# Kernel optimization log

Hardware: AMD Instinct MI355X
Metric: run time of the kernel (lower is better)

The kernel has to match this reference:

```python
import jax, jax.numpy as jnp
import numpy as np

HIDDEN = 128
GRID = 8
NB = 32.0            # neighborhood_size
CELL = NB / GRID      # cell_size


def setup_inputs() -> dict:
    key = jax.random.key(0)
    k1, k2, k3, k4 = jax.random.split(key, 4)
    N = 1024
    hidden_states = jax.random.normal(k1, (N, HIDDEN), dtype=jnp.float32)
    positions = jax.random.uniform(k2, (N, 2), dtype=jnp.float32) * 100.0
    fan_in = GRID * GRID * HIDDEN
    bound = 1.0 / np.sqrt(fan_in)
    W = jax.random.uniform(k3, (fan_in, HIDDEN), dtype=jnp.float32, minval=-bound, maxval=bound)
    b = jax.random.uniform(k4, (HIDDEN,), dtype=jnp.float32, minval=-bound, maxval=bound)
    return {"hidden_states": hidden_states, "positions": positions, "W": W, "b": b}


def reference(hidden_states, positions, W, b):
    N, H = hidden_states.shape
    G = GRID
    pos = jax.lax.stop_gradient(positions)  # indices carry no gradient (matches torch int())
    # rel[i, j] = positions[j] - positions[i]
    rel = pos[None, :, :] - pos[:, None, :]                      # [N, N, 2]
    half = NB / 2.0
    inside = (jnp.abs(rel[..., 0]) <= half) & (jnp.abs(rel[..., 1]) <= half)
    not_self = ~jnp.eye(N, dtype=bool)
    valid = inside & not_self                                     # [N, N]
    # rel + half is in [0, NB] when inside, so floor == int() truncation
    gx = jnp.clip(jnp.floor((rel[..., 0] + half) / CELL).astype(jnp.int32), 0, G - 1)
    gy = jnp.clip(jnp.floor((rel[..., 1] + half) / CELL).astype(jnp.int32), 0, G - 1)
    cell = gy * G + gx                                            # [N, N], in [0, G*G)
    # invalid pairs go to a dummy cell G*G per pedestrian
    seg = jnp.where(valid, cell, G * G)
    gid = (jnp.arange(N, dtype=jnp.int32)[:, None] * (G * G + 1) + seg).reshape(-1)
    data = jnp.broadcast_to(hidden_states[None, :, :], (N, N, H)).reshape(N * N, H)
    gmax = jax.ops.segment_max(data, gid, num_segments=N * (G * G + 1))  # [N*(G*G+1), H]
    # torch grid starts at zeros and uses maximum -> clamp at 0; empty cells (-inf) -> 0
    grid = jnp.maximum(gmax.reshape(N, G * G + 1, H)[:, : G * G, :], 0.0)  # [N, G*G, H]
    flat = grid.reshape(N, G * G * H)
    return flat @ W + b
```

## Files before the change

kernel.cpp:

```cpp
#include <hip/hip_runtime.h>
#include <hip/hip_bf16.h>

#define N_PED 1024
#define H 128
#define G 8
#define NCELL 64
#define K_TOT 8192
#define HALF_NB 16.0f
#define INV_CELL 0.25f

#define KSPLIT 16
#define KC 512
#define BM 64
#define BK 64
#define NSTAGE 8

typedef __attribute__((ext_vector_type(8))) short bf16x8;
typedef __attribute__((ext_vector_type(4))) float f32x4;

__device__ __forceinline__ unsigned map_f2u(float v) {
    unsigned u = __float_as_uint(v);
    return (u & 0x80000000u) ? ~u : (u | 0x80000000u);
}
__device__ __forceinline__ unsigned pack2x(unsigned ua, unsigned ub) {
    float2 f = {__uint_as_float(ua ^ 0x80000000u),
                __uint_as_float(ub ^ 0x80000000u)};
    union { __hip_bfloat162 h; unsigned u; } cv;
    cv.h = __float22bfloat162_rn(f);
    return cv.u;
}
__device__ __forceinline__ unsigned pack2f(float fa, float fb) {
    float2 f = {fa, fb};
    union { __hip_bfloat162 h; unsigned u; } cv;
    cv.h = __float22bfloat162_rn(f);
    return cv.u;
}
__device__ __forceinline__ void gl_lds16(const void* g, void* l) {
    __builtin_amdgcn_global_load_lds(
        (const __attribute__((address_space(1))) void*)g,
        (__attribute__((address_space(3))) void*)l, 16, 0, 0);
}

__global__ __launch_bounds__(512) void fused_pre(const float* __restrict__ hs,
                                                 const float* __restrict__ pos,
                                                 const float* __restrict__ W,
                                                 ushort* __restrict__ grid,
                                                 ushort* __restrict__ Wt) {
    __shared__ __align__(16) char smem[36872];
    const int tid = threadIdx.x;

    if (blockIdx.x < N_PED) {
        unsigned* lgrid = (unsigned*)smem;
        int*      list  = (int*)(smem + 32768);
        int*      cnt   = (int*)(smem + 36864);
        const int i = blockIdx.x;

        const unsigned iu = 0x80000000u;
        uint4 iv = {iu, iu, iu, iu};
        for (int k = tid; k < NCELL * H / 4; k += 512) ((uint4*)lgrid)[k] = iv;
        if (tid == 0) *cnt = 0;
        __syncthreads();

        const float2 pi = ((const float2*)pos)[i];
        for (int j = tid; j < N_PED; j += 512) {
            float2 pj = ((const float2*)pos)[j];
            float rx = pj.x - pi.x;
            float ry = pj.y - pi.y;
            if (j != i && fabsf(rx) <= HALF_NB && fabsf(ry) <= HALF_NB) {
                int gx = min(G - 1, max(0, (int)floorf((rx + HALF_NB) * INV_CELL)));
                int gy = min(G - 1, max(0, (int)floorf((ry + HALF_NB) * INV_CELL)));
                int slot = atomicAdd(cnt, 1);
                list[slot] = (j << 8) | (gy * G + gx);
            }
        }
        __syncthreads();

        const int n  = *cnt;
        const int c  = tid & 31;
        const int eg = tid >> 5;
        int e  = eg;
        int p0 = (e < n) ? list[e] : -1;
        int p1 = (e + 16 < n) ? list[e + 16] : -1;
        float v0[4] = {};
        if (p0 >= 0) {
            const float* hp = &hs[(p0 >> 8) * H + c];
            v0[0] = hp[0]; v0[1] = hp[32]; v0[2] = hp[64]; v0[3] = hp[96];
        }
        while (p0 >= 0) {
            int p2 = (e + 32 < n) ? list[e + 32] : -1;
            float v1[4] = {};
            if (p1 >= 0) {
                const float* hp = &hs[(p1 >> 8) * H + c];
                v1[0] = hp[0]; v1[1] = hp[32]; v1[2] = hp[64]; v1[3] = hp[96];
            }
            unsigned* gph = &lgrid[(p0 & 255) * H + c];
            atomicMax(gph + 0,  map_f2u(v0[0]));
            atomicMax(gph + 32, map_f2u(v0[1]));
            atomicMax(gph + 64, map_f2u(v0[2]));
            atomicMax(gph + 96, map_f2u(v0[3]));
            e += 16; p0 = p1; p1 = p2;
            v0[0] = v1[0]; v0[1] = v1[1]; v0[2] = v1[2]; v0[3] = v1[3];
        }
        __syncthreads();

        uint2* dst2 = (uint2*)(grid + (size_t)i * K_TOT);
        for (int q = tid; q < K_TOT / 4; q += 512) {
            uint4 a = ((const uint4*)lgrid)[q];
            uint2 o;
            o.x = pack2x(a.x, a.y);
            o.y = pack2x(a.z, a.w);
            dst2[q] = o;
        }
    } else {
        float* tile = (float*)smem;
        const int bw  = blockIdx.x - N_PED;
        const int k0w = bw * 64;

        for (int x = tid; x < 64 * H; x += 512) {
            int r = x >> 7, cc = x & 127;
            tile[r * 129 + cc] = W[(size_t)(k0w + r) * H + cc];
        }
        __syncthreads();

        const int col = tid >> 2;
        const int kh  = (tid & 3) * 16;
        uint tmp[8];
        #pragma unroll
        for (int t = 0; t < 8; ++t)
            tmp[t] = pack2f(tile[(kh + 2 * t) * 129 + col],
                            tile[(kh + 2 * t + 1) * 129 + col]);
        uint4* w0 = (uint4*)(Wt + (size_t)col * K_TOT + k0w + kh);
        w0[0] = *(const uint4*)&tmp[0];
        w0[1] = *(const uint4*)&tmp[4];
    }
}

__global__ __launch_bounds__(512) void gemm_mfma(const ushort* __restrict__ A,
                                                 const ushort* __restrict__ Wt,
                                                 float* __restrict__ part) {
    __shared__ ushort sA[3][BM * BK];
    __shared__ ushort sB[3][H * BK];

    const int bx = blockIdx.x;
    const int mx = 2 * (bx & 7) + ((bx >> 3) & 1);
    const int ky = bx >> 4;
    const int m0 = mx * BM;
    const int k0 = ky * KC;

    const int tid  = threadIdx.x;
    const int wave = tid >> 6;
    const int lane = tid & 63;
    const int ll   = lane & 15;
    const int lh   = lane >> 4;
    const int lr8  = lane >> 3;
    const int cswz = (lane & 7) ^ (lr8 & 7);
    const int wr   = wave >> 2;
    const int wc   = wave & 3;

    const ushort* Abase = A  + (size_t)(m0 + 8 * wave + lr8) * K_TOT + k0 + cswz * 8;
    const ushort* Bbase = Wt + (size_t)(16 * wave + lr8) * K_TOT     + k0 + cswz * 8;

    f32x4 acc[2][2] = {};

#define STAGE(T, BUF)                                                          \
    do {                                                                       \
        gl_lds16(Abase + (T) * BK, &sA[BUF][(8 * wave) * BK]);                 \
        gl_lds16(Bbase + (T) * BK,              &sB[BUF][(16 * wave) * BK]);   \
        gl_lds16(Bbase + (T) * BK + 8 * K_TOT,  &sB[BUF][(16 * wave + 8) * BK]); \
    } while (0)

    STAGE(0, 0);
    STAGE(1, 1);
    asm volatile("s_waitcnt vmcnt(3)" ::: "memory");
    __builtin_amdgcn_s_barrier();

    #pragma unroll
    for (int t = 0; t < NSTAGE; ++t) {
        if (t + 2 < NSTAGE) STAGE(t + 2, (t + 2) % 3);

        const int buf = t % 3;
        #pragma unroll
        for (int ks = 0; ks < 2; ++ks) {
            const int ch = ks * 4 + lh;
            bf16x8 afrag[2], bfrag[2];
            #pragma unroll
            for (int mt = 0; mt < 2; ++mt) {
                int ar = wr * 32 + mt * 16 + ll;
                afrag[mt] = *(const bf16x8*)&sA[buf][ar * BK + ((ch ^ (ar & 7)) * 8)];
            }
            #pragma unroll
            for (int nt = 0; nt < 2; ++nt) {
                int br = wc * 32 + nt * 16 + ll;
                bfrag[nt] = *(const bf16x8*)&sB[buf][br * BK + ((ch ^ (br & 7)) * 8)];
            }
            #pragma unroll
            for (int mt = 0; mt < 2; ++mt)
                #pragma unroll
                for (int nt = 0; nt < 2; ++nt)
                    acc[mt][nt] = __builtin_amdgcn_mfma_f32_16x16x32_bf16(
                        afrag[mt], bfrag[nt], acc[mt][nt], 0, 0, 0);
        }

        if (t + 1 < NSTAGE) {
            if (t + 2 < NSTAGE)
                asm volatile("s_waitcnt vmcnt(3)" ::: "memory");
            else
                asm volatile("s_waitcnt vmcnt(0)" ::: "memory");
            __builtin_amdgcn_s_barrier();
        }
    }
#undef STAGE

    float* dst = part + (size_t)ky * (N_PED * H);
    #pragma unroll
    for (int mt = 0; mt < 2; ++mt)
        #pragma unroll
        for (int nt = 0; nt < 2; ++nt) {
            int col   = wc * 32 + nt * 16 + ll;
            int rbase = m0 + wr * 32 + mt * 16 + lh * 4;
            #pragma unroll
            for (int r = 0; r < 4; ++r)
                dst[(size_t)(rbase + r) * H + col] = acc[mt][nt][r];
        }
}

__global__ __launch_bounds__(128) void reduce_out(const float* __restrict__ part,
                                                  const float* __restrict__ b,
                                                  float* __restrict__ out) {
    const int idx = (blockIdx.x * 128 + threadIdx.x) * 4;
    float4 acc = *(const float4*)&b[idx & (H - 1)];
    #pragma unroll
    for (int s = 0; s < KSPLIT; ++s) {
        float4 p = *(const float4*)&part[(size_t)s * (N_PED * H) + idx];
        acc.x += p.x; acc.y += p.y; acc.z += p.z; acc.w += p.w;
    }
    *(float4*)&out[idx] = acc;
}

extern "C" void kernel_launch(void* const* d_in, const int* in_sizes, int n_in,
                              void* d_out, int out_size, void* d_ws, size_t ws_size,
                              hipStream_t stream) {
    const float* hs  = (const float*)d_in[0];
    const float* pos = (const float*)d_in[1];
    const float* Wm  = (const float*)d_in[2];
    const float* b   = (const float*)d_in[3];
    float* out = (float*)d_out;

    ushort* grid = (ushort*)d_ws;
    ushort* Wt   = (ushort*)((char*)d_ws + (16u << 20));
    float*  part = (float*)((char*)d_ws + (18u << 20));

    fused_pre<<<N_PED + 128, 512, 0, stream>>>(hs, pos, Wm, grid, Wt);
    gemm_mfma<<<KSPLIT * (N_PED / BM), 512, 0, stream>>>(grid, Wt, part);
    reduce_out<<<(N_PED * H) / (128 * 4), 128, 0, stream>>>(part, b, out);
}
```

Before: 29.28 us.

## Fuse grid max-pooling into split-K GEMM and replace dense grid with neighbor lists

The prep kernel now only builds compact per-pedestrian neighbor lists (16 pedestrians per block) plus the transposed bf16 W. It no longer materializes the dense 16 MB bf16 grid. The GEMM kernel filters each list down to the cells belonging to its K-chunk and max-pools hidden states into LDS. It then packs the result to bf16 in a swizzled A tile and runs MFMA directly, which removes the global write and read of the grid. In exchange, list capacities (LISTCAP 192, MCAP 160) silently truncate overly dense neighborhoods. Occupancy also drops because the kernel uses about 66 KB of LDS, and there is no double-buffered pipelining across the four sub-steps.

Result: slower. 49.10 us (+67.7%).

```diff
diff --git a/kernel.cpp b/kernel.cpp
--- a/kernel.cpp
+++ b/kernel.cpp
@@ -4,16 +4,13 @@
 #define N_PED 1024
 #define H 128
 #define G 8
-#define NCELL 64
 #define K_TOT 8192
 #define HALF_NB 16.0f
 #define INV_CELL 0.25f
-
+#define LISTCAP 192
+#define MCAP 160
 #define KSPLIT 16
-#define KC 512
 #define BM 64
-#define BK 64
-#define NSTAGE 8
 
 typedef __attribute__((ext_vector_type(8))) short bf16x8;
 typedef __attribute__((ext_vector_type(4))) float f32x4;
@@ -41,87 +38,48 @@
         (__attribute__((address_space(3))) void*)l, 16, 0, 0);
 }
 
-__global__ __launch_bounds__(512) void fused_pre(const float* __restrict__ hs,
-                                                 const float* __restrict__ pos,
-                                                 const float* __restrict__ W,
-                                                 ushort* __restrict__ grid,
-                                                 ushort* __restrict__ Wt) {
-    __shared__ __align__(16) char smem[36872];
+__global__ __launch_bounds__(512) void prep(const float* __restrict__ pos,
+                                            const float* __restrict__ W,
+                                            ushort* __restrict__ lists,
+                                            int* __restrict__ cntg,
+                                            ushort* __restrict__ Wt) {
+    __shared__ __align__(16) char smem[33024];
     const int tid = threadIdx.x;
 
-    if (blockIdx.x < N_PED) {
-        unsigned* lgrid = (unsigned*)smem;
-        int*      list  = (int*)(smem + 32768);
-        int*      cnt   = (int*)(smem + 36864);
-        const int i = blockIdx.x;
-
-        const unsigned iu = 0x80000000u;
-        uint4 iv = {iu, iu, iu, iu};
-        for (int k = tid; k < NCELL * H / 4; k += 512) ((uint4*)lgrid)[k] = iv;
-        if (tid == 0) *cnt = 0;
-        __syncthreads();
-
-        const float2 pi = ((const float2*)pos)[i];
+    if (blockIdx.x < 64) {
+        float2* pis  = (float2*)smem;
+        int*    lcnt = (int*)(smem + 128);
+        ushort* ll   = (ushort*)(smem + 192);
+        const int base = blockIdx.x * 16;
+        if (tid < 16) { pis[tid] = ((const float2*)pos)[base + tid]; lcnt[tid] = 0; }
+        __syncthreads();
         for (int j = tid; j < N_PED; j += 512) {
             float2 pj = ((const float2*)pos)[j];
-            float rx = pj.x - pi.x;
-            float ry = pj.y - pi.y;
-            if (j != i && fabsf(rx) <= HALF_NB && fabsf(ry) <= HALF_NB) {
-                int gx = min(G - 1, max(0, (int)floorf((rx + HALF_NB) * INV_CELL)));
-                int gy = min(G - 1, max(0, (int)floorf((ry + HALF_NB) * INV_CELL)));
-                int slot = atomicAdd(cnt, 1);
-                list[slot] = (j << 8) | (gy * G + gx);
+            #pragma unroll
+            for (int p = 0; p < 16; ++p) {
+                float rx = pj.x - pis[p].x;
+                float ry = pj.y - pis[p].y;
+                if (j != base + p && fabsf(rx) <= HALF_NB && fabsf(ry) <= HALF_NB) {
+                    int gx = min(G - 1, max(0, (int)floorf((rx + HALF_NB) * INV_CELL)));
+                    int gy = min(G - 1, max(0, (int)floorf((ry + HALF_NB) * INV_CELL)));
+                    int slot = atomicAdd(&lcnt[p], 1);
+                    if (slot < LISTCAP) ll[p * LISTCAP + slot] = (ushort)((j << 6) | (gy * G + gx));
+                }
             }
         }
         __syncthreads();
-
-        const int n  = *cnt;
-        const int c  = tid & 31;
-        const int eg = tid >> 5;
-        int e  = eg;
-        int p0 = (e < n) ? list[e] : -1;
-        int p1 = (e + 16 < n) ? list[e + 16] : -1;
-        float v0[4] = {};
-        if (p0 >= 0) {
-            const float* hp = &hs[(p0 >> 8) * H + c];
-            v0[0] = hp[0]; v0[1] = hp[32]; v0[2] = hp[64]; v0[3] = hp[96];
-        }
-        while (p0 >= 0) {
-            int p2 = (e + 32 < n) ? list[e + 32] : -1;
-            float v1[4] = {};
-            if (p1 >= 0) {
-                const float* hp = &hs[(p1 >> 8) * H + c];
-                v1[0] = hp[0]; v1[1] = hp[32]; v1[2] = hp[64]; v1[3] = hp[96];
-            }
-            unsigned* gph = &lgrid[(p0 & 255) * H + c];
-            atomicMax(gph + 0,  map_f2u(v0[0]));
-            atomicMax(gph + 32, map_f2u(v0[1]));
-            atomicMax(gph + 64, map_f2u(v0[2]));
-            atomicMax(gph + 96, map_f2u(v0[3]));
-            e += 16; p0 = p1; p1 = p2;
-            v0[0] = v1[0]; v0[1] = v1[1]; v0[2] = v1[2]; v0[3] = v1[3];
-        }
-        __syncthreads();
-
-        uint2* dst2 = (uint2*)(grid + (size_t)i * K_TOT);
-        for (int q = tid; q < K_TOT / 4; q += 512) {
-            uint4 a = ((const uint4*)lgrid)[q];
-            uint2 o;
-            o.x = pack2x(a.x, a.y);
-            o.y = pack2x(a.z, a.w);
-            dst2[q] = o;
-        }
+        uint4* dst = (uint4*)(lists + (size_t)base * LISTCAP);
+        for (int x = tid; x < 16 * LISTCAP / 8; x += 512) dst[x] = ((const uint4*)ll)[x];
+        if (tid < 16) cntg[base + tid] = min(lcnt[tid], LISTCAP);
     } else {
         float* tile = (float*)smem;
-        const int bw  = blockIdx.x - N_PED;
+        const int bw  = blockIdx.x - 64;
         const int k0w = bw * 64;
-
         for (int x = tid; x < 64 * H; x += 512) {
             int r = x >> 7, cc = x & 127;
             tile[r * 129 + cc] = W[(size_t)(k0w + r) * H + cc];
         }
         __syncthreads();
-
         const int col = tid >> 2;
         const int kh  = (tid & 3) * 16;
         uint tmp[8];
@@ -135,88 +93,164 @@
     }
 }
 
-__global__ __launch_bounds__(512) void gemm_mfma(const ushort* __restrict__ A,
-                                                 const ushort* __restrict__ Wt,
-                                                 float* __restrict__ part) {
-    __shared__ ushort sA[3][BM * BK];
-    __shared__ ushort sB[3][H * BK];
-
-    const int bx = blockIdx.x;
-    const int mx = 2 * (bx & 7) + ((bx >> 3) & 1);
-    const int ky = bx >> 4;
+__global__ __launch_bounds__(512, 4) void pool_gemm(const float* __restrict__ hs,
+                                                    const ushort* __restrict__ lists,
+                                                    const int* __restrict__ cntg,
+                                                    const ushort* __restrict__ Wt,
+                                                    float* __restrict__ part) {
+    __shared__ __align__(16) char smem[66832];
+    uint*   pool = (uint*)smem;
+    ushort* Alds = (ushort*)smem;
+    char*   Bb   = smem + 32768;
+    ushort* ml   = (ushort*)(smem + 65536);
+    int*    mcnt = (int*)(smem + 65536 + 4 * MCAP * 2);
+
+    const int mx = blockIdx.x, ky = blockIdx.y;
     const int m0 = mx * BM;
-    const int k0 = ky * KC;
-
+    const int kbase = ky * 512;
     const int tid  = threadIdx.x;
-    const int wave = tid >> 6;
-    const int lane = tid & 63;
-    const int ll   = lane & 15;
-    const int lh   = lane >> 4;
-    const int lr8  = lane >> 3;
+    const int wave = tid >> 6, lane = tid & 63;
+    const int ll_  = lane & 15, lh = lane >> 4, lr8 = lane >> 3;
     const int cswz = (lane & 7) ^ (lr8 & 7);
-    const int wr   = wave >> 2;
-    const int wc   = wave & 3;
-
-    const ushort* Abase = A  + (size_t)(m0 + 8 * wave + lr8) * K_TOT + k0 + cswz * 8;
-    const ushort* Bbase = Wt + (size_t)(16 * wave + lr8) * K_TOT     + k0 + cswz * 8;
+    const int wr = wave >> 2, wc = wave & 3;
+
+    const int p_own = tid >> 3, su = tid & 7;
+    const uint4* lp = (const uint4*)(lists + (size_t)(m0 + p_own) * LISTCAP);
+    uint4 le0 = lp[su];
+    uint4 le1 = lp[su + 8];
+    uint4 le2 = lp[su + 16];
+    const int np = cntg[m0 + p_own];
+    if (tid < 4) mcnt[tid] = 0;
+    __syncthreads();
+
+#define COMPACT_U4(LE, IBASE)                                                  \
+    {                                                                          \
+        _Pragma("unroll")                                                      \
+        for (int s = 0; s < 8; ++s) {                                          \
+            uint w = ((const uint*)&(LE))[s >> 1];                             \
+            ushort ent = (s & 1) ? (ushort)(w >> 16) : (ushort)(w & 0xFFFFu);  \
+            int idx = (IBASE) + s;                                             \
+            if (idx < np) {                                                    \
+                int cell = ent & 63;                                           \
+                if ((cell >> 2) == ky) {                                       \
+                    int q = cell & 3;                                          \
+                    int slot = atomicAdd(&mcnt[q], 1);                         \
+                    if (slot < MCAP)                                           \
+                        ml[q * MCAP + slot] =                                  \
+                            (ushort)((((int)ent >> 6) << 6) | p_own);          \
+                }                                                              \
+            }                                                                  \
+        }                                                                      \
+    }
+    COMPACT_U4(le0, su * 8)
+    COMPACT_U4(le1, (su + 8) * 8)
+    COMPACT_U4(le2, (su + 16) * 8)
+#undef COMPACT_U4
+    __syncthreads();
+    int nq[4];
+    nq[0] = min(mcnt[0], MCAP); nq[1] = min(mcnt[1], MCAP);
+    nq[2] = min(mcnt[2], MCAP); nq[3] = min(mcnt[3], MCAP);
 
     f32x4 acc[2][2] = {};
 
-#define STAGE(T, BUF)                                                          \
-    do {                                                                       \
-        gl_lds16(Abase + (T) * BK, &sA[BUF][(8 * wave) * BK]);                 \
-        gl_lds16(Bbase + (T) * BK,              &sB[BUF][(16 * wave) * BK]);   \
-        gl_lds16(Bbase + (T) * BK + 8 * K_TOT,  &sB[BUF][(16 * wave + 8) * BK]); \
-    } while (0)
-
-    STAGE(0, 0);
-    STAGE(1, 1);
-    asm volatile("s_waitcnt vmcnt(3)" ::: "memory");
-    __builtin_amdgcn_s_barrier();
-
     #pragma unroll
-    for (int t = 0; t < NSTAGE; ++t) {
-        if (t + 2 < NSTAGE) STAGE(t + 2, (t + 2) % 3);
-
-        const int buf = t % 3;
+    for (int q = 0; q < 4; ++q) {
+        {
+            const ushort* Bs = Wt + kbase + q * 128 + cswz * 8;
+            const size_t r0 = (size_t)(16 * wave + lr8) * K_TOT;
+            const size_t r1 = (size_t)(16 * wave + 8 + lr8) * K_TOT;
+            gl_lds16(Bs + r0,      Bb + (16 * wave) * 128);
+            gl_lds16(Bs + r1,      Bb + (16 * wave + 8) * 128);
+            gl_lds16(Bs + r0 + 64, Bb + 16384 + (16 * wave) * 128);
+            gl_lds16(Bs + r1 + 64, Bb + 16384 + (16 * wave + 8) * 128);
+        }
+        {
+            uint4 iv = {0x80000000u, 0x80000000u, 0x80000000u, 0x80000000u};
+            uint4* P4 = (uint4*)pool;
+            #pragma unroll
+            for (int r = 0; r < 4; ++r) P4[tid + r * 512] = iv;
+        }
+        __syncthreads();
+
+        {
+            const int dim = tid & 127;
+            const int eg  = tid >> 7;
+            const int n   = nq[q];
+            int e  = eg;
+            int p0 = (e < n)     ? (int)ml[q * MCAP + e]     : -1;
+            int p1 = (e + 4 < n) ? (int)ml[q * MCAP + e + 4] : -1;
+            float v0 = 0.f;
+            if (p0 >= 0) v0 = hs[(size_t)(p0 >> 6) * H + dim];
+            while (p0 >= 0) {
+                int p2 = (e + 8 < n) ? (int)ml[q * MCAP + e + 8] : -1;
+                float v1 = 0.f;
+                if (p1 >= 0) v1 = hs[(size_t)(p1 >> 6) * H + dim];
+                atomicMax(&pool[(p0 & 63) * H + dim], map_f2u(v0));
+                e += 4; p0 = p1; p1 = p2; v0 = v1;
+            }
+        }
+        __syncthreads();
+
+        uint4 c0a, c0b, c1a, c1b;
+        {
+            const uint4* P4 = (const uint4*)pool;
+            const int cid0 = tid, cid1 = tid + 512;
+            c0a = P4[(cid0 >> 4) * 32 + (cid0 & 15) * 2];
+            c0b = P4[(cid0 >> 4) * 32 + (cid0 & 15) * 2 + 1];
+            c1a = P4[(cid1 >> 4) * 32 + (cid1 & 15) * 2];
+            c1b = P4[(cid1 >> 4) * 32 + (cid1 & 15) * 2 + 1];
+        }
+        __syncthreads();
+        {
+            const int cid0 = tid, cid1 = tid + 512;
+            uint4 o0, o1;
+            o0.x = pack2x(c0a.x, c0a.y); o0.y = pack2x(c0a.z, c0a.w);
+            o0.z = pack2x(c0b.x, c0b.y); o0.w = pack2x(c0b.z, c0b.w);
+            o1.x = pack2x(c1a.x, c1a.y); o1.y = pack2x(c1a.z, c1a.w);
+            o1.z = pack2x(c1b.x, c1b.y); o1.w = pack2x(c1b.z, c1b.w);
+            int p0 = cid0 >> 4, ch0 = cid0 & 15;
+            int p1 = cid1 >> 4, ch1 = cid1 & 15;
+            *(uint4*)((char*)Alds + p0 * 256 + ((ch0 ^ (p0 & 15)) * 16)) = o0;
+            *(uint4*)((char*)Alds + p1 * 256 + ((ch1 ^ (p1 & 15)) * 16)) = o1;
+        }
+        __syncthreads();
+
         #pragma unroll
-        for (int ks = 0; ks < 2; ++ks) {
-            const int ch = ks * 4 + lh;
-            bf16x8 afrag[2], bfrag[2];
-            #pragma unroll
-            for (int mt = 0; mt < 2; ++mt) {
-                int ar = wr * 32 + mt * 16 + ll;
-                afrag[mt] = *(const bf16x8*)&sA[buf][ar * BK + ((ch ^ (ar & 7)) * 8)];
+        for (int h = 0; h < 2; ++h) {
+            #pragma unroll
+            for (int ks = 0; ks < 2; ++ks) {
+                const int gch = h * 8 + ks * 4 + lh;
+                const int ch  = ks * 4 + lh;
+                bf16x8 af[2], bf[2];
+                #pragma unroll
+                for (int mt = 0; mt < 2; ++mt) {
+                    int ar = wr * 32 + mt * 16 + ll_;
+                    af[mt] = *(const bf16x8*)((const char*)Alds + ar * 256 +
+                                              ((gch ^ (ar & 15)) * 16));
+                }
+                #pragma unroll
+                for (int nt = 0; nt < 2; ++nt) {
+                    int br = wc * 32 + nt * 16 + ll_;
+                    bf[nt] = *(const bf16x8*)(Bb + h * 16384 + br * 128 +
+                                              ((ch ^ (br & 7)) * 16));
+                }
+                #pragma unroll
+                for (int mt = 0; mt < 2; ++mt)
+                    #pragma unroll
+                    for (int nt = 0; nt < 2; ++nt)
+                        acc[mt][nt] = __builtin_amdgcn_mfma_f32_16x16x32_bf16(
+                            af[mt], bf[nt], acc[mt][nt], 0, 0, 0);
             }
-            #pragma unroll
-            for (int nt = 0; nt < 2; ++nt) {
-                int br = wc * 32 + nt * 16 + ll;
-                bfrag[nt] = *(const bf16x8*)&sB[buf][br * BK + ((ch ^ (br & 7)) * 8)];
-            }
-            #pragma unroll
-            for (int mt = 0; mt < 2; ++mt)
-                #pragma unroll
-                for (int nt = 0; nt < 2; ++nt)
-                    acc[mt][nt] = __builtin_amdgcn_mfma_f32_16x16x32_bf16(
-                        afrag[mt], bfrag[nt], acc[mt][nt], 0, 0, 0);
-        }
-
-        if (t + 1 < NSTAGE) {
-            if (t + 2 < NSTAGE)
-                asm volatile("s_waitcnt vmcnt(3)" ::: "memory");
-            else
-                asm volatile("s_waitcnt vmcnt(0)" ::: "memory");
-            __builtin_amdgcn_s_barrier();
-        }
-    }
-#undef STAGE
+        }
+        __syncthreads();
+    }
 
     float* dst = part + (size_t)ky * (N_PED * H);
     #pragma unroll
     for (int mt = 0; mt < 2; ++mt)
         #pragma unroll
         for (int nt = 0; nt < 2; ++nt) {
-            int col   = wc * 32 + nt * 16 + ll;
+            int col   = wc * 32 + nt * 16 + ll_;
             int rbase = m0 + wr * 32 + mt * 16 + lh * 4;
             #pragma unroll
             for (int r = 0; r < 4; ++r)
@@ -246,11 +280,12 @@
     const float* b   = (const float*)d_in[3];
     float* out = (float*)d_out;
 
-    ushort* grid = (ushort*)d_ws;
-    ushort* Wt   = (ushort*)((char*)d_ws + (16u << 20));
-    float*  part = (float*)((char*)d_ws + (18u << 20));
-
-    fused_pre<<<N_PED + 128, 512, 0, stream>>>(hs, pos, Wm, grid, Wt);
-    gemm_mfma<<<KSPLIT * (N_PED / BM), 512, 0, stream>>>(grid, Wt, part);
+    ushort* Wt    = (ushort*)d_ws;
+    ushort* lists = (ushort*)((char*)d_ws + (2u << 20));
+    int*    cntg  = (int*)((char*)d_ws + (2u << 20) + (512u << 10));
+    float*  part  = (float*)((char*)d_ws + (3u << 20));
+
+    prep<<<192, 512, 0, stream>>>(pos, Wm, lists, cntg, Wt);
+    pool_gemm<<<dim3(16, 16), 512, 0, stream>>>(hs, lists, cntg, Wt, part);
     reduce_out<<<(N_PED * H) / (128 * 4), 128, 0, stream>>>(part, b, out);
 }
```
